# Kernel tuning notes

Measured on AMD Instinct MI355X. Metric: run time of the kernel, lower is better.

Reference implementation:

```python
import jax, jax.numpy as jnp
import numpy as np

T, N, I, H, OUT = 16, 4096, 4, 32, 1


def setup_inputs() -> dict:
    key = jax.random.key(0)
    ks = jax.random.split(key, 12)
    f32 = jnp.float32
    x_path = jax.random.normal(ks[0], (T, N, I), f32)
    adj = jax.random.normal(ks[1], (N, N), f32) / np.float32(np.sqrt(N))
    W_enc = jax.random.normal(ks[2], (I, H), f32) / np.float32(np.sqrt(I))
    b_enc = jnp.zeros((H,), f32)
    W_gcn = jax.random.normal(ks[3], (H, H), f32) / np.float32(np.sqrt(H))
    b_gcn = jnp.zeros((H,), f32)
    W_time = jax.random.normal(ks[4], (H, H), f32) / np.float32(np.sqrt(H))
    b_time = jnp.zeros((H,), f32)
    W_proj = jax.random.normal(ks[5], (H, H * I), f32) * np.float32(0.1 / np.sqrt(H))
    b_proj = jnp.zeros((H * I,), f32)
    W_d1 = jax.random.normal(ks[6], (H, 16), f32) / np.float32(np.sqrt(H))
    b_d1 = jnp.zeros((16,), f32)
    W_d2 = jax.random.normal(ks[7], (16, OUT), f32) / np.float32(4.0)
    b_d2 = jnp.zeros((OUT,), f32)
    return dict(x_path=x_path, adj=adj, W_enc=W_enc, b_enc=b_enc,
                W_gcn=W_gcn, b_gcn=b_gcn, W_time=W_time, b_time=b_time,
                W_proj=W_proj, b_proj=b_proj, W_d1=W_d1, b_d1=b_d1,
                W_d2=W_d2, b_d2=b_d2)


def _natural_cubic_coeffs(y):
    # y: (T, C) samples on uniform grid t=0..T-1 (h=1).
    # Natural cubic spline: tridiagonal solve for second derivatives M.
    Tn = y.shape[0]
    main = jnp.ones((Tn,), y.dtype).at[1:-1].set(4.0)
    A = jnp.diag(main)
    idx = jnp.arange(1, Tn - 1)
    A = A.at[idx, idx - 1].set(1.0).at[idx, idx + 1].set(1.0)
    rhs = jnp.zeros_like(y).at[1:-1].set(6.0 * (y[2:] - 2.0 * y[1:-1] + y[:-2]))
    M = jnp.linalg.solve(A, rhs)
    b = (y[1:] - y[:-1]) - (2.0 * M[:-1] + M[1:]) / 6.0
    c = M[:-1] / 2.0
    d = (M[1:] - M[:-1]) / 6.0
    return b, c, d  # each (T-1, C); dX/dt on interval i at local s: b+2cs+3ds^2


def reference(x_path, adj, W_enc, b_enc, W_gcn, b_gcn, W_time, b_time,
              W_proj, b_proj, W_d1, b_d1, W_d2, b_d2):
    Tn, Nn, In = x_path.shape
    Hn = W_enc.shape[1]
    y = x_path.reshape(Tn, Nn * In)
    sb, sc, sd = _natural_cubic_coeffs(y)

    # z0 = encoder(X(t0)); spline value at grid point 0 equals the sample.
    z0 = x_path[0] @ W_enc + b_enc  # (N, H)

    def vf(z, dxdt):
        # SpatialVectorField + projector + block-diagonal Jacobian applied to dX/dt.
        # z: (N, H), dxdt: (N, I)
        zn = adj @ z                                     # GCN neighbor aggregation
        h = jax.nn.relu(zn @ W_gcn + b_gcn + z @ W_time + b_time)
        sens = (h @ W_proj + b_proj).reshape(Nn, Hn, In)  # per-site Jacobian blocks
        # site_identity * sens -> block-diag; matmul with dX reduces to per-site contraction
        return jnp.einsum('nhi,ni->nh', sens, dxdt)

    def rk4_step(z, coefs):
        bi, ci, di = coefs  # (N*I,)
        def dxdt(s):
            return (bi + 2.0 * ci * s + 3.0 * di * s * s).reshape(Nn, In)
        k1 = vf(z, dxdt(0.0))
        k2 = vf(z + 0.5 * k1, dxdt(0.5))
        k3 = vf(z + 0.5 * k2, dxdt(0.5))
        k4 = vf(z + k3, dxdt(1.0))
        zn = z + (k1 + 2.0 * k2 + 2.0 * k3 + k4) / 6.0
        return zn, zn

    _, zs = jax.lax.scan(rk4_step, z0, (sb, sc, sd))
    zT = jnp.concatenate([z0[None], zs], axis=0)  # (T, N, H)

    hdec = jax.nn.relu(zT @ W_d1 + b_d1)
    return jax.nn.sigmoid(hdec @ W_d2 + b_d2)  # (T, N, OUT)
```

## Files before the change

kernel.cpp:

```cpp
#include <hip/hip_runtime.h>
#include <hip/hip_bf16.h>

#define NN 4096
#define NI 16384
#define HH 32

typedef __attribute__((ext_vector_type(8))) short short8;
typedef __attribute__((ext_vector_type(4))) float f32x4;

__device__ __forceinline__ short f2bs(float f) {
  __hip_bfloat16 b = __float2bfloat16(f);
  return *(short*)&b;
}

__global__ __launch_bounds__(512) void k_cvt(const float* __restrict__ a,
                                             short* __restrict__ ab) {
  const int tid = threadIdx.x;
  const int W = tid >> 6, lane = tid & 63;
  const int fr = lane & 15, oct = lane >> 4;
  const int R = blockIdx.x;
  const float* srow = a + (long)(R * 16 + fr) * NN + W * 512 + oct * 8;
  short* drow = ab + ((long)(R * 8 + W) * 16) * 512 + lane * 8;
#pragma unroll 4
  for (int i = 0; i < 16; ++i) {
    const float4 u0 = *(const float4*)(srow + i * 32);
    const float4 u1 = *(const float4*)(srow + i * 32 + 4);
    short8 r;
    r[0] = f2bs(u0.x); r[1] = f2bs(u0.y); r[2] = f2bs(u0.z); r[3] = f2bs(u0.w);
    r[4] = f2bs(u1.x); r[5] = f2bs(u1.y); r[6] = f2bs(u1.z); r[7] = f2bs(u1.w);
    *(short8*)(drow + i * 512) = r;
  }
}

__device__ __forceinline__ long zt_idx(int n, int h) {
  const int hb = h >> 4, hl = h & 15;
  const int kb = n >> 5, oct = (n >> 3) & 3, j = n & 7;
  return ((long)(hb * 128 + kb) * 64 + hl + 16 * oct) * 8 + j;
}

__global__ void k_spline(const float* __restrict__ x,
                         float* __restrict__ dx0, float* __restrict__ dxh,
                         float* __restrict__ dx1) {
  const int c = blockIdx.x * 256 + threadIdx.x;
  float y[16];
#pragma unroll
  for (int t = 0; t < 16; ++t) y[t] = x[t * NI + c];
  float cp[15], dp[15], M[16];
  cp[1] = 0.25f;
  dp[1] = (6.f * (y[2] - 2.f * y[1] + y[0])) * 0.25f;
#pragma unroll
  for (int i = 2; i <= 14; ++i) {
    float ri = 6.f * (y[i + 1] - 2.f * y[i] + y[i - 1]);
    float inv = 1.f / (4.f - cp[i - 1]);
    cp[i] = inv;
    dp[i] = (ri - dp[i - 1]) * inv;
  }
  M[0] = 0.f; M[15] = 0.f;
  M[14] = dp[14];
#pragma unroll
  for (int i = 13; i >= 1; --i) M[i] = dp[i] - cp[i] * M[i + 1];
#pragma unroll
  for (int i = 0; i < 15; ++i) {
    float b = (y[i + 1] - y[i]) - (2.f * M[i] + M[i + 1]) * (1.f / 6.f);
    float cc = 0.5f * M[i];
    float dd = (M[i + 1] - M[i]) * (1.f / 6.f);
    dx0[i * NI + c] = b;
    dxh[i * NI + c] = b + cc + 0.75f * dd;
    dx1[i * NI + c] = b + 2.f * cc + 3.f * dd;
  }
}

__global__ void k_enc(const float* __restrict__ x,
                      const float* __restrict__ We,
                      const float* __restrict__ be,
                      float* __restrict__ zcur, float* __restrict__ ze,
                      short* __restrict__ zT) {
  const int g = blockIdx.x * 256 + threadIdx.x;
  const int n = g >> 5, h = g & 31;
  float acc = be[h];
#pragma unroll
  for (int i = 0; i < 4; ++i) acc = fmaf(x[n * 4 + i], We[i * 32 + h], acc);
  zcur[g] = acc;
  ze[g] = acc;
  zT[zt_idx(n, h)] = f2bs(acc);
}

__global__ void k_dec0(const float* __restrict__ z,
                       const float* __restrict__ W1,
                       const float* __restrict__ b1,
                       const float* __restrict__ W2,
                       const float* __restrict__ b2,
                       float* __restrict__ out) {
  __shared__ float W1s[32][17];
  __shared__ float b1s[16], W2s[16], b2s;
  const int tid = threadIdx.x;
  for (int idx = tid; idx < 512; idx += 256) W1s[idx >> 4][idx & 15] = W1[idx];
  if (tid < 16) { b1s[tid] = b1[tid]; W2s[tid] = W2[tid]; }
  if (tid == 0) b2s = b2[0];
  __syncthreads();
  const int n = blockIdx.x * 256 + tid;
  const float* zr = z + (long)n * 32;
  float zv[32];
#pragma unroll
  for (int hh = 0; hh < 32; ++hh) zv[hh] = zr[hh];
  float acc = b2s;
#pragma unroll
  for (int jj = 0; jj < 16; ++jj) {
    float hv = b1s[jj];
#pragma unroll
    for (int hh = 0; hh < 32; ++hh) hv = fmaf(zv[hh], W1s[hh][jj], hv);
    acc = fmaf(fmaxf(hv, 0.f), W2s[jj], acc);
  }
  out[n] = 1.f / (1.f + expf(-acc));
}

__global__ __launch_bounds__(512) void k_vf(
    const short* __restrict__ adjb,
    const short* __restrict__ zT_in,
    short* __restrict__ zT_out,
    float* __restrict__ z_eval,
    const float* __restrict__ z_base,
    float* __restrict__ z_next,
    float* __restrict__ kout,
    const float* __restrict__ k1, const float* __restrict__ k2,
    const float* __restrict__ k3,
    const float* __restrict__ dxsel,
    const float* __restrict__ Wg, const float* __restrict__ bg,
    const float* __restrict__ Wt, const float* __restrict__ bt,
    const float* __restrict__ Wp, const float* __restrict__ bp,
    const float* __restrict__ Wd1, const float* __restrict__ bd1,
    const float* __restrict__ Wd2, const float* __restrict__ bd2,
    float* __restrict__ out, int out_base, int j) {
  __shared__ float red[8][16][32];
  __shared__ float zn_s[16][32];
  __shared__ float h_s[16][32];
  __shared__ float ze_s[16][32];
  __shared__ float Wg_s[32][32];
  __shared__ float Wt_s[32][32];
  __shared__ float Wp_s[32][132];
  __shared__ float Wd1_s[32][16];
  __shared__ float bgt_s[32];
  __shared__ float bp_s[128];
  __shared__ float dsm[33];

  const int tid = threadIdx.x;
  const int lane = tid & 63;
  const int w = tid >> 6;
  const int r0 = blockIdx.x * 16;

  for (int idx = tid; idx < 1024; idx += 512) {
    Wg_s[idx >> 5][idx & 31] = Wg[idx];
    Wt_s[idx >> 5][idx & 31] = Wt[idx];
  }
  for (int idx = tid; idx < 4096; idx += 512)
    Wp_s[idx >> 7][idx & 127] = Wp[idx];
  if (tid < 32) bgt_s[tid] = bg[tid] + bt[tid];
  if (tid < 128) bp_s[tid] = bp[tid];
  ze_s[tid >> 5][tid & 31] = z_eval[r0 * 32 + tid];
  if (j == 4) {
    Wd1_s[tid >> 4 & 31][tid & 15] = (tid < 512) ? Wd1[tid] : 0.f;
    if (tid < 16) { dsm[tid] = bd1[tid]; dsm[16 + tid] = Wd2[tid]; }
    if (tid == 0) dsm[32] = bd2[0];
  }

  f32x4 acc0 = {0.f, 0.f, 0.f, 0.f};
  f32x4 acc1 = {0.f, 0.f, 0.f, 0.f};
  const short* ap = adjb + ((long)(blockIdx.x * 8 + w) * 16) * 512 + lane * 8;
  const short* b0p = zT_in + ((long)(w * 16)) * 512 + lane * 8;
  const short* b1p = zT_in + ((long)(128 + w * 16)) * 512 + lane * 8;
#pragma unroll 8
  for (int i = 0; i < 16; ++i) {
    const short8 a  = *(const short8*)(ap + i * 512);
    const short8 b0 = *(const short8*)(b0p + i * 512);
    const short8 b1 = *(const short8*)(b1p + i * 512);
    acc0 = __builtin_amdgcn_mfma_f32_16x16x32_bf16(a, b0, acc0, 0, 0, 0);
    acc1 = __builtin_amdgcn_mfma_f32_16x16x32_bf16(a, b1, acc1, 0, 0, 0);
  }
  {
    const int crow = (lane >> 4) * 4;
    const int ccol = lane & 15;
#pragma unroll
    for (int q = 0; q < 4; ++q) {
      red[w][crow + q][ccol] = acc0[q];
      red[w][crow + q][ccol + 16] = acc1[q];
    }
  }
  __syncthreads();

  const int r = tid >> 5, c = tid & 31;
  {
    float zn = 0.f;
#pragma unroll
    for (int q = 0; q < 8; ++q) zn += red[q][r][c];
    zn_s[r][c] = zn;
  }
  __syncthreads();

  {
    float hv = bgt_s[c];
#pragma unroll
    for (int kk = 0; kk < 32; ++kk)
      hv = fmaf(zn_s[r][kk], Wg_s[kk][c], fmaf(ze_s[r][kk], Wt_s[kk][c], hv));
    h_s[r][c] = fmaxf(hv, 0.f);
  }
  __syncthreads();

  {
    const long row = r0 + r;
    float kv = 0.f;
#pragma unroll
    for (int i = 0; i < 4; ++i) {
      float s = bp_s[c * 4 + i];
#pragma unroll
      for (int hp = 0; hp < 32; ++hp) s = fmaf(h_s[r][hp], Wp_s[hp][c * 4 + i], s);
      kv = fmaf(s, dxsel[row * 4 + i], kv);
    }
    const long g = row * 32 + c;
    float znew;
    if (j == 4) {
      znew = z_base[g] + (k1[g] + 2.f * k2[g] + 2.f * k3[g] + kv) * (1.f / 6.f);
      z_next[g] = znew;
      zn_s[r][c] = znew;
    } else {
      kout[g] = kv;
      znew = z_base[g] + ((j == 3) ? 1.f : 0.5f) * kv;
    }
    z_eval[g] = znew;
    zT_out[zt_idx((int)row, c)] = f2bs(znew);
  }

  if (j == 4) {
    __syncthreads();
    if (tid < 16) {
      float acc = dsm[32];
#pragma unroll
      for (int jj = 0; jj < 16; ++jj) {
        float hv = dsm[jj];
#pragma unroll
        for (int hh = 0; hh < 32; ++hh) hv = fmaf(zn_s[tid][hh], Wd1_s[hh][jj], hv);
        acc = fmaf(fmaxf(hv, 0.f), dsm[16 + jj], acc);
      }
      out[out_base + r0 + tid] = 1.f / (1.f + expf(-acc));
    }
  }
}

extern "C" void kernel_launch(void* const* d_in, const int* in_sizes, int n_in,
                              void* d_out, int out_size, void* d_ws, size_t ws_size,
                              hipStream_t stream) {
  (void)in_sizes; (void)n_in; (void)out_size; (void)ws_size;
  const float* x      = (const float*)d_in[0];
  const float* adj    = (const float*)d_in[1];
  const float* W_enc  = (const float*)d_in[2];
  const float* b_enc  = (const float*)d_in[3];
  const float* W_gcn  = (const float*)d_in[4];
  const float* b_gcn  = (const float*)d_in[5];
  const float* W_time = (const float*)d_in[6];
  const float* b_time = (const float*)d_in[7];
  const float* W_proj = (const float*)d_in[8];
  const float* b_proj = (const float*)d_in[9];
  const float* W_d1   = (const float*)d_in[10];
  const float* b_d1   = (const float*)d_in[11];
  const float* W_d2   = (const float*)d_in[12];
  const float* b_d2   = (const float*)d_in[13];
  float* out = (float*)d_out;

  float* dx0   = (float*)d_ws;
  float* dxh   = dx0 + 15 * NI;
  float* dx1   = dxh + 15 * NI;
  float* zcur  = dx1 + 15 * NI;
  float* znext = zcur + NN * HH;
  float* zev   = znext + NN * HH;
  float* k1b   = zev + NN * HH;
  float* k2b   = k1b + NN * HH;
  float* k3b   = k2b + NN * HH;
  short* zTa   = (short*)(k3b + NN * HH);
  short* zTb   = zTa + HH * NN;
  short* adjb  = zTb + HH * NN;

  k_cvt<<<256, 512, 0, stream>>>(adj, adjb);
  k_spline<<<64, 256, 0, stream>>>(x, dx0, dxh, dx1);
  k_enc<<<512, 256, 0, stream>>>(x, W_enc, b_enc, zcur, zev, zTa);
  k_dec0<<<16, 256, 0, stream>>>(zcur, W_d1, b_d1, W_d2, b_d2, out);

  short* zin = zTa;
  short* zout = zTb;
  for (int t = 0; t < 15; ++t) {
    const float* ds[4] = { dx0 + t * NI, dxh + t * NI, dxh + t * NI, dx1 + t * NI };
    for (int j = 1; j <= 4; ++j) {
      float* ko = (j == 1) ? k1b : (j == 2) ? k2b : k3b;
      k_vf<<<256, 512, 0, stream>>>(adjb, zin, zout, zev, zcur, znext, ko,
                                    k1b, k2b, k3b, ds[j - 1],
                                    W_gcn, b_gcn, W_time, b_time, W_proj, b_proj,
                                    W_d1, b_d1, W_d2, b_d2, out, (t + 1) * NN, j);
      short* tmp = zin; zin = zout; zout = tmp;
    }
    float* tz = zcur; zcur = znext; znext = tz;
  }
}
```

Measured before the change: 810.4 us.

## Fuse all RK4 stages into one persistent cooperative kernel with grid barriers

Replaces the 60 per-stage kernel launches, along with the separate conversion, encoder and decoder kernels, with a single persistent cooperative kernel that loops over all stages. Stages are separated by a custom grid barrier built on atomic counters. Each block converts its 16 rows of the adjacency matrix to bf16 once and keeps them in LDS (128 KB) for the whole run. RK4 intermediates stay in registers instead of global buffers. This removes launch overhead and repeated adjacency reads from HBM, but adds barrier latency and reduces occupancy to one 256-thread block per CU.

```diff
diff --git a/kernel.cpp b/kernel.cpp
--- a/kernel.cpp
+++ b/kernel.cpp
@@ -12,24 +12,9 @@
   __hip_bfloat16 b = __float2bfloat16(f);
   return *(short*)&b;
 }
-
-__global__ __launch_bounds__(512) void k_cvt(const float* __restrict__ a,
-                                             short* __restrict__ ab) {
-  const int tid = threadIdx.x;
-  const int W = tid >> 6, lane = tid & 63;
-  const int fr = lane & 15, oct = lane >> 4;
-  const int R = blockIdx.x;
-  const float* srow = a + (long)(R * 16 + fr) * NN + W * 512 + oct * 8;
-  short* drow = ab + ((long)(R * 8 + W) * 16) * 512 + lane * 8;
-#pragma unroll 4
-  for (int i = 0; i < 16; ++i) {
-    const float4 u0 = *(const float4*)(srow + i * 32);
-    const float4 u1 = *(const float4*)(srow + i * 32 + 4);
-    short8 r;
-    r[0] = f2bs(u0.x); r[1] = f2bs(u0.y); r[2] = f2bs(u0.z); r[3] = f2bs(u0.w);
-    r[4] = f2bs(u1.x); r[5] = f2bs(u1.y); r[6] = f2bs(u1.z); r[7] = f2bs(u1.w);
-    *(short8*)(drow + i * 512) = r;
-  }
+__device__ __forceinline__ float bs2f(short s) {
+  __hip_bfloat16 b = *(__hip_bfloat16*)&s;
+  return __bfloat162float(b);
 }
 
 __device__ __forceinline__ long zt_idx(int n, int h) {
@@ -40,8 +25,9 @@
 
 __global__ void k_spline(const float* __restrict__ x,
                          float* __restrict__ dx0, float* __restrict__ dxh,
-                         float* __restrict__ dx1) {
+                         float* __restrict__ dx1, unsigned* __restrict__ bar) {
   const int c = blockIdx.x * 256 + threadIdx.x;
+  if (blockIdx.x == 0) { bar[threadIdx.x] = 0u; bar[threadIdx.x + 256] = 0u; }
   float y[16];
 #pragma unroll
   for (int t = 0; t < 16; ++t) y[t] = x[t * NI + c];
@@ -70,75 +56,49 @@
   }
 }
 
-__global__ void k_enc(const float* __restrict__ x,
-                      const float* __restrict__ We,
-                      const float* __restrict__ be,
-                      float* __restrict__ zcur, float* __restrict__ ze,
-                      short* __restrict__ zT) {
-  const int g = blockIdx.x * 256 + threadIdx.x;
-  const int n = g >> 5, h = g & 31;
-  float acc = be[h];
-#pragma unroll
-  for (int i = 0; i < 4; ++i) acc = fmaf(x[n * 4 + i], We[i * 32 + h], acc);
-  zcur[g] = acc;
-  ze[g] = acc;
-  zT[zt_idx(n, h)] = f2bs(acc);
-}
-
-__global__ void k_dec0(const float* __restrict__ z,
-                       const float* __restrict__ W1,
-                       const float* __restrict__ b1,
-                       const float* __restrict__ W2,
-                       const float* __restrict__ b2,
-                       float* __restrict__ out) {
-  __shared__ float W1s[32][17];
-  __shared__ float b1s[16], W2s[16], b2s;
-  const int tid = threadIdx.x;
-  for (int idx = tid; idx < 512; idx += 256) W1s[idx >> 4][idx & 15] = W1[idx];
-  if (tid < 16) { b1s[tid] = b1[tid]; W2s[tid] = W2[tid]; }
-  if (tid == 0) b2s = b2[0];
+struct OdeP {
+  const float *x, *We, *be, *adj;
+  const float *Wg, *bg, *Wt, *bt, *Wp, *bp, *Wd1, *bd1, *Wd2, *bd2;
+  const float *dx0, *dxh, *dx1;
+  short *zTa, *zTb;
+  float *out;
+  unsigned *bar;
+};
+
+__device__ __forceinline__ void gbar(const OdeP& p, int bar_i, int bid) {
   __syncthreads();
-  const int n = blockIdx.x * 256 + tid;
-  const float* zr = z + (long)n * 32;
-  float zv[32];
-#pragma unroll
-  for (int hh = 0; hh < 32; ++hh) zv[hh] = zr[hh];
-  float acc = b2s;
-#pragma unroll
-  for (int jj = 0; jj < 16; ++jj) {
-    float hv = b1s[jj];
-#pragma unroll
-    for (int hh = 0; hh < 32; ++hh) hv = fmaf(zv[hh], W1s[hh][jj], hv);
-    acc = fmaf(fmaxf(hv, 0.f), W2s[jj], acc);
-  }
-  out[n] = 1.f / (1.f + expf(-acc));
-}
-
-__global__ __launch_bounds__(512) void k_vf(
-    const short* __restrict__ adjb,
-    const short* __restrict__ zT_in,
-    short* __restrict__ zT_out,
-    float* __restrict__ z_eval,
-    const float* __restrict__ z_base,
-    float* __restrict__ z_next,
-    float* __restrict__ kout,
-    const float* __restrict__ k1, const float* __restrict__ k2,
-    const float* __restrict__ k3,
-    const float* __restrict__ dxsel,
-    const float* __restrict__ Wg, const float* __restrict__ bg,
-    const float* __restrict__ Wt, const float* __restrict__ bt,
-    const float* __restrict__ Wp, const float* __restrict__ bp,
-    const float* __restrict__ Wd1, const float* __restrict__ bd1,
-    const float* __restrict__ Wd2, const float* __restrict__ bd2,
-    float* __restrict__ out, int out_base, int j) {
-  __shared__ float red[8][16][32];
-  __shared__ float zn_s[16][32];
-  __shared__ float h_s[16][32];
-  __shared__ float ze_s[16][32];
+  if (threadIdx.x == 0) {
+    __threadfence();
+    __hip_atomic_fetch_add(&p.bar[(bid & 7) * 32], 1u,
+                           __ATOMIC_RELAXED, __HIP_MEMORY_SCOPE_AGENT);
+    const unsigned tgt = (unsigned)(bar_i + 1);
+    if (bid == 0) {
+#pragma unroll 1
+      for (int s2 = 0; s2 < 8; ++s2)
+        while (__hip_atomic_load(&p.bar[s2 * 32], __ATOMIC_RELAXED,
+                                 __HIP_MEMORY_SCOPE_AGENT) < tgt * 32u)
+          __builtin_amdgcn_s_sleep(1);
+      __threadfence();
+      __hip_atomic_store(&p.bar[256], tgt, __ATOMIC_RELAXED, __HIP_MEMORY_SCOPE_AGENT);
+    } else {
+      while (__hip_atomic_load(&p.bar[256], __ATOMIC_RELAXED,
+                               __HIP_MEMORY_SCOPE_AGENT) < tgt)
+        __builtin_amdgcn_s_sleep(1);
+    }
+  }
+  __syncthreads();
+  __threadfence();
+}
+
+__global__ __launch_bounds__(256, 1) void k_ode(OdeP p) {
+  __shared__ __align__(16) short adjs[65536];
+  __shared__ float zn_s[16][33];
+  __shared__ float ze_s[16][33];
+  __shared__ float h_s[16][33];
   __shared__ float Wg_s[32][32];
   __shared__ float Wt_s[32][32];
-  __shared__ float Wp_s[32][132];
-  __shared__ float Wd1_s[32][16];
+  __shared__ float Wp_s[32][128];
+  __shared__ short Wd1_s[512];
   __shared__ float bgt_s[32];
   __shared__ float bp_s[128];
   __shared__ float dsm[33];
@@ -146,102 +106,173 @@
   const int tid = threadIdx.x;
   const int lane = tid & 63;
   const int w = tid >> 6;
-  const int r0 = blockIdx.x * 16;
-
-  for (int idx = tid; idx < 1024; idx += 512) {
-    Wg_s[idx >> 5][idx & 31] = Wg[idx];
-    Wt_s[idx >> 5][idx & 31] = Wt[idx];
-  }
-  for (int idx = tid; idx < 4096; idx += 512)
-    Wp_s[idx >> 7][idx & 127] = Wp[idx];
-  if (tid < 32) bgt_s[tid] = bg[tid] + bt[tid];
-  if (tid < 128) bp_s[tid] = bp[tid];
-  ze_s[tid >> 5][tid & 31] = z_eval[r0 * 32 + tid];
-  if (j == 4) {
-    Wd1_s[tid >> 4 & 31][tid & 15] = (tid < 512) ? Wd1[tid] : 0.f;
-    if (tid < 16) { dsm[tid] = bd1[tid]; dsm[16 + tid] = Wd2[tid]; }
-    if (tid == 0) dsm[32] = bd2[0];
-  }
-
-  f32x4 acc0 = {0.f, 0.f, 0.f, 0.f};
-  f32x4 acc1 = {0.f, 0.f, 0.f, 0.f};
-  const short* ap = adjb + ((long)(blockIdx.x * 8 + w) * 16) * 512 + lane * 8;
-  const short* b0p = zT_in + ((long)(w * 16)) * 512 + lane * 8;
-  const short* b1p = zT_in + ((long)(128 + w * 16)) * 512 + lane * 8;
-#pragma unroll 8
-  for (int i = 0; i < 16; ++i) {
-    const short8 a  = *(const short8*)(ap + i * 512);
-    const short8 b0 = *(const short8*)(b0p + i * 512);
-    const short8 b1 = *(const short8*)(b1p + i * 512);
-    acc0 = __builtin_amdgcn_mfma_f32_16x16x32_bf16(a, b0, acc0, 0, 0, 0);
-    acc1 = __builtin_amdgcn_mfma_f32_16x16x32_bf16(a, b1, acc1, 0, 0, 0);
-  }
+  const int bid = blockIdx.x;
+  const int r0 = bid * 16;
+  const int lane8 = lane * 8;
+  const int fr = lane & 15, oct = lane >> 4;
+
+  for (int idx = tid; idx < 1024; idx += 256) {
+    Wg_s[idx >> 5][idx & 31] = p.Wg[idx];
+    Wt_s[idx >> 5][idx & 31] = p.Wt[idx];
+  }
+  for (int idx = tid; idx < 4096; idx += 256) ((float*)Wp_s)[idx] = p.Wp[idx];
+  for (int idx = tid; idx < 512; idx += 256) Wd1_s[idx] = f2bs(p.Wd1[idx]);
+  if (tid < 32) bgt_s[tid] = p.bg[tid] + p.bt[tid];
+  if (tid < 128) bp_s[tid] = p.bp[tid];
+  if (tid < 16) { dsm[tid] = p.bd1[tid]; dsm[16 + tid] = p.Wd2[tid]; }
+  if (tid == 0) dsm[32] = p.bd2[0];
+
   {
-    const int crow = (lane >> 4) * 4;
-    const int ccol = lane & 15;
-#pragma unroll
-    for (int q = 0; q < 4; ++q) {
-      red[w][crow + q][ccol] = acc0[q];
-      red[w][crow + q][ccol + 16] = acc1[q];
-    }
+    const float* srow = p.adj + (long)(r0 + fr) * NN + w * 1024 + oct * 8;
+#pragma unroll 4
+    for (int i = 0; i < 32; ++i) {
+      const float4 u0 = *(const float4*)(srow + i * 32);
+      const float4 u1 = *(const float4*)(srow + i * 32 + 4);
+      short8 r;
+      r[0] = f2bs(u0.x); r[1] = f2bs(u0.y); r[2] = f2bs(u0.z); r[3] = f2bs(u0.w);
+      r[4] = f2bs(u1.x); r[5] = f2bs(u1.y); r[6] = f2bs(u1.z); r[7] = f2bs(u1.w);
+      *(short8*)&adjs[(w * 32 + i) * 512 + lane8] = r;
+    }
+  }
+
+  float zb[2], k1r[2] = {0.f, 0.f}, k2r[2] = {0.f, 0.f}, k3r[2] = {0.f, 0.f};
+#pragma unroll
+  for (int e = 0; e < 2; ++e) {
+    const int idx = tid + e * 256;
+    const int r = idx >> 5, c = idx & 31;
+    const int n = r0 + r;
+    const float4 xv = *(const float4*)&p.x[n * 4];
+    float z0 = p.be[c];
+    z0 = fmaf(xv.x, p.We[0 * 32 + c], z0);
+    z0 = fmaf(xv.y, p.We[1 * 32 + c], z0);
+    z0 = fmaf(xv.z, p.We[2 * 32 + c], z0);
+    z0 = fmaf(xv.w, p.We[3 * 32 + c], z0);
+    zb[e] = z0;
+    ze_s[r][c] = z0;
+    h_s[r][c] = z0;
+    zn_s[r][c] = 0.f;
+    p.zTa[zt_idx(n, c)] = f2bs(z0);
   }
   __syncthreads();
 
-  const int r = tid >> 5, c = tid & 31;
-  {
-    float zn = 0.f;
-#pragma unroll
-    for (int q = 0; q < 8; ++q) zn += red[q][r][c];
-    zn_s[r][c] = zn;
-  }
-  __syncthreads();
-
-  {
-    float hv = bgt_s[c];
-#pragma unroll
-    for (int kk = 0; kk < 32; ++kk)
-      hv = fmaf(zn_s[r][kk], Wg_s[kk][c], fmaf(ze_s[r][kk], Wt_s[kk][c], hv));
-    h_s[r][c] = fmaxf(hv, 0.f);
-  }
-  __syncthreads();
-
-  {
-    const long row = r0 + r;
-    float kv = 0.f;
-#pragma unroll
-    for (int i = 0; i < 4; ++i) {
-      float s = bp_s[c * 4 + i];
-#pragma unroll
-      for (int hp = 0; hp < 32; ++hp) s = fmaf(h_s[r][hp], Wp_s[hp][c * 4 + i], s);
-      kv = fmaf(s, dxsel[row * 4 + i], kv);
-    }
-    const long g = row * 32 + c;
-    float znew;
+  if (tid < 16) {
+    float acc = dsm[32];
+#pragma unroll
+    for (int jj = 0; jj < 16; ++jj) {
+      float hv = dsm[jj];
+#pragma unroll
+      for (int hh = 0; hh < 32; ++hh) hv = fmaf(h_s[tid][hh], bs2f(Wd1_s[hh * 16 + jj]), hv);
+      acc = fmaf(fmaxf(hv, 0.f), dsm[16 + jj], acc);
+    }
+    p.out[r0 + tid] = 1.f / (1.f + expf(-acc));
+  }
+
+  int bar_i = 0;
+  gbar(p, bar_i++, bid);
+
+  const int fb = w * 32;
+#pragma unroll 1
+  for (int s = 0; s < 60; ++s) {
+    const int t = s >> 2;
+    const int j = (s & 3) + 1;
+    const short* zi = (s & 1) ? p.zTb : p.zTa;
+    short* zo = (s & 1) ? p.zTa : p.zTb;
+    const float* dxp = (j == 1) ? (p.dx0 + t * NI)
+                     : (j == 4) ? (p.dx1 + t * NI) : (p.dxh + t * NI);
+
+    f32x4 a0 = {0.f,0.f,0.f,0.f}, a1 = {0.f,0.f,0.f,0.f};
+    f32x4 a2 = {0.f,0.f,0.f,0.f}, a3 = {0.f,0.f,0.f,0.f};
+#pragma unroll 4
+    for (int i = 0; i < 32; i += 2) {
+      const int f0 = fb + i, f1 = fb + i + 1;
+      const short8 av0 = *(const short8*)&adjs[f0 * 512 + lane8];
+      const short8 bv00 = *(const short8*)(zi + (long)f0 * 512 + lane8);
+      const short8 bv01 = *(const short8*)(zi + (long)(128 + f0) * 512 + lane8);
+      const short8 av1 = *(const short8*)&adjs[f1 * 512 + lane8];
+      const short8 bv10 = *(const short8*)(zi + (long)f1 * 512 + lane8);
+      const short8 bv11 = *(const short8*)(zi + (long)(128 + f1) * 512 + lane8);
+      a0 = __builtin_amdgcn_mfma_f32_16x16x32_bf16(av0, bv00, a0, 0, 0, 0);
+      a1 = __builtin_amdgcn_mfma_f32_16x16x32_bf16(av0, bv01, a1, 0, 0, 0);
+      a2 = __builtin_amdgcn_mfma_f32_16x16x32_bf16(av1, bv10, a2, 0, 0, 0);
+      a3 = __builtin_amdgcn_mfma_f32_16x16x32_bf16(av1, bv11, a3, 0, 0, 0);
+    }
+    const f32x4 acc0 = a0 + a2, acc1 = a1 + a3;
+    {
+      const int crow = (lane >> 4) * 4;
+      const int ccol = lane & 15;
+#pragma unroll
+      for (int q = 0; q < 4; ++q) {
+        atomicAdd(&zn_s[crow + q][ccol], acc0[q]);
+        atomicAdd(&zn_s[crow + q][ccol + 16], acc1[q]);
+      }
+    }
+    __syncthreads();
+
+#pragma unroll
+    for (int e = 0; e < 2; ++e) {
+      const int idx = tid + e * 256;
+      const int r = idx >> 5, c = idx & 31;
+      float hv = bgt_s[c];
+#pragma unroll
+      for (int kk = 0; kk < 32; ++kk)
+        hv = fmaf(zn_s[r][kk], Wg_s[kk][c], fmaf(ze_s[r][kk], Wt_s[kk][c], hv));
+      h_s[r][c] = fmaxf(hv, 0.f);
+    }
+    __syncthreads();
+
+    float znew[2];
+#pragma unroll
+    for (int e = 0; e < 2; ++e) {
+      const int idx = tid + e * 256;
+      const int r = idx >> 5, c = idx & 31;
+      const int row = r0 + r;
+      const float4 dxv = *(const float4*)&dxp[row * 4];
+      float kv = 0.f;
+#pragma unroll
+      for (int i = 0; i < 4; ++i) {
+        float sv = bp_s[c * 4 + i];
+#pragma unroll
+        for (int hp = 0; hp < 32; ++hp) sv = fmaf(h_s[r][hp], Wp_s[hp][c * 4 + i], sv);
+        const float dx = (i == 0) ? dxv.x : (i == 1) ? dxv.y : (i == 2) ? dxv.z : dxv.w;
+        kv = fmaf(sv, dx, kv);
+      }
+      float zn2;
+      if (j == 4) {
+        zn2 = zb[e] + (k1r[e] + 2.f * k2r[e] + 2.f * k3r[e] + kv) * (1.f / 6.f);
+        zb[e] = zn2;
+      } else {
+        if (j == 1) k1r[e] = kv; else if (j == 2) k2r[e] = kv; else k3r[e] = kv;
+        zn2 = zb[e] + ((j == 3) ? 1.f : 0.5f) * kv;
+      }
+      znew[e] = zn2;
+      zn_s[r][c] = 0.f;
+      ze_s[r][c] = zn2;
+      zo[zt_idx(row, c)] = f2bs(zn2);
+    }
+
     if (j == 4) {
-      znew = z_base[g] + (k1[g] + 2.f * k2[g] + 2.f * k3[g] + kv) * (1.f / 6.f);
-      z_next[g] = znew;
-      zn_s[r][c] = znew;
-    } else {
-      kout[g] = kv;
-      znew = z_base[g] + ((j == 3) ? 1.f : 0.5f) * kv;
-    }
-    z_eval[g] = znew;
-    zT_out[zt_idx((int)row, c)] = f2bs(znew);
-  }
-
-  if (j == 4) {
-    __syncthreads();
-    if (tid < 16) {
-      float acc = dsm[32];
-#pragma unroll
-      for (int jj = 0; jj < 16; ++jj) {
-        float hv = dsm[jj];
-#pragma unroll
-        for (int hh = 0; hh < 32; ++hh) hv = fmaf(zn_s[tid][hh], Wd1_s[hh][jj], hv);
-        acc = fmaf(fmaxf(hv, 0.f), dsm[16 + jj], acc);
-      }
-      out[out_base + r0 + tid] = 1.f / (1.f + expf(-acc));
-    }
+      __syncthreads();
+#pragma unroll
+      for (int e = 0; e < 2; ++e) {
+        const int idx = tid + e * 256;
+        h_s[idx >> 5][idx & 31] = znew[e];
+      }
+      __syncthreads();
+      if (tid < 16) {
+        float acc = dsm[32];
+#pragma unroll
+        for (int jj = 0; jj < 16; ++jj) {
+          float hv = dsm[jj];
+#pragma unroll
+          for (int hh = 0; hh < 32; ++hh)
+            hv = fmaf(h_s[tid][hh], bs2f(Wd1_s[hh * 16 + jj]), hv);
+          acc = fmaf(fmaxf(hv, 0.f), dsm[16 + jj], acc);
+        }
+        p.out[(t + 1) * NN + r0 + tid] = 1.f / (1.f + expf(-acc));
+      }
+    }
+
+    if (s < 59) gbar(p, bar_i++, bid);
   }
 }
 
@@ -263,38 +294,29 @@
   const float* b_d1   = (const float*)d_in[11];
   const float* W_d2   = (const float*)d_in[12];
   const float* b_d2   = (const float*)d_in[13];
-  float* out = (float*)d_out;
-
-  float* dx0   = (float*)d_ws;
-  float* dxh   = dx0 + 15 * NI;
-  float* dx1   = dxh + 15 * NI;
-  float* zcur  = dx1 + 15 * NI;
-  float* znext = zcur + NN * HH;
-  float* zev   = znext + NN * HH;
-  float* k1b   = zev + NN * HH;
-  float* k2b   = k1b + NN * HH;
-  float* k3b   = k2b + NN * HH;
-  short* zTa   = (short*)(k3b + NN * HH);
-  short* zTb   = zTa + HH * NN;
-  short* adjb  = zTb + HH * NN;
-
-  k_cvt<<<256, 512, 0, stream>>>(adj, adjb);
-  k_spline<<<64, 256, 0, stream>>>(x, dx0, dxh, dx1);
-  k_enc<<<512, 256, 0, stream>>>(x, W_enc, b_enc, zcur, zev, zTa);
-  k_dec0<<<16, 256, 0, stream>>>(zcur, W_d1, b_d1, W_d2, b_d2, out);
-
-  short* zin = zTa;
-  short* zout = zTb;
-  for (int t = 0; t < 15; ++t) {
-    const float* ds[4] = { dx0 + t * NI, dxh + t * NI, dxh + t * NI, dx1 + t * NI };
-    for (int j = 1; j <= 4; ++j) {
-      float* ko = (j == 1) ? k1b : (j == 2) ? k2b : k3b;
-      k_vf<<<256, 512, 0, stream>>>(adjb, zin, zout, zev, zcur, znext, ko,
-                                    k1b, k2b, k3b, ds[j - 1],
-                                    W_gcn, b_gcn, W_time, b_time, W_proj, b_proj,
-                                    W_d1, b_d1, W_d2, b_d2, out, (t + 1) * NN, j);
-      short* tmp = zin; zin = zout; zout = tmp;
-    }
-    float* tz = zcur; zcur = znext; znext = tz;
-  }
-}
+
+  unsigned* bar = (unsigned*)d_ws;
+  float* dx0 = (float*)(bar + 512);
+  float* dxh = dx0 + 15 * NI;
+  float* dx1 = dxh + 15 * NI;
+  short* zTa = (short*)(dx1 + 15 * NI);
+  short* zTb = zTa + HH * NN;
+
+  k_spline<<<64, 256, 0, stream>>>(x, dx0, dxh, dx1, bar);
+
+  OdeP p;
+  p.x = x; p.We = W_enc; p.be = b_enc; p.adj = adj;
+  p.Wg = W_gcn; p.bg = b_gcn; p.Wt = W_time; p.bt = b_time;
+  p.Wp = W_proj; p.bp = b_proj; p.Wd1 = W_d1; p.bd1 = b_d1;
+  p.Wd2 = W_d2; p.bd2 = b_d2;
+  p.dx0 = dx0; p.dxh = dxh; p.dx1 = dx1;
+  p.zTa = zTa; p.zTb = zTb;
+  p.out = (float*)d_out; p.bar = bar;
+
+  void* args[] = { &p };
+  hipError_t rc = hipLaunchCooperativeKernel((const void*)k_ode, dim3(256), dim3(256),
+                                             args, 0, stream);
+  if (rc != hipSuccess) {
+    k_ode<<<256, 256, 0, stream>>>(p);
+  }
+}
```

After: 2.304 ms. 2.84x slower.

## Double k_vf block to 16 waves, issue MFMA loads before weight staging

Applied to the files above, without the earlier changes.

The vector-field kernel now launches 1024 threads per block, so 16 waves each handle half as many K-chunks of the adjacency matmul, and the partial results are reduced through a padded shared buffer. The adjacency and state loads are issued before the weight staging to shared memory, so the global latency overlaps with it. The projection stage now loads h into registers and reads Wp as float4. The intent is to hide memory latency in this latency-bound, launch-heavy step. The cost is a larger reduction and half of the threads sitting idle in the epilogue stages.

```diff
diff --git a/kernel.cpp b/kernel.cpp
--- a/kernel.cpp
+++ b/kernel.cpp
@@ -114,7 +114,7 @@
   out[n] = 1.f / (1.f + expf(-acc));
 }
 
-__global__ __launch_bounds__(512) void k_vf(
+__global__ __launch_bounds__(1024) void k_vf(
     const short* __restrict__ adjb,
     const short* __restrict__ zT_in,
     short* __restrict__ zT_out,
@@ -131,13 +131,13 @@
     const float* __restrict__ Wd1, const float* __restrict__ bd1,
     const float* __restrict__ Wd2, const float* __restrict__ bd2,
     float* __restrict__ out, int out_base, int j) {
-  __shared__ float red[8][16][32];
-  __shared__ float zn_s[16][32];
-  __shared__ float h_s[16][32];
-  __shared__ float ze_s[16][32];
+  __shared__ float red2[16][32][17];
+  __shared__ float zn_s[16][33];
+  __shared__ float h_s[16][33];
+  __shared__ float ze_s[16][33];
   __shared__ float Wg_s[32][32];
   __shared__ float Wt_s[32][32];
-  __shared__ float Wp_s[32][132];
+  __shared__ float Wp_s[32][136];
   __shared__ float Wd1_s[32][16];
   __shared__ float bgt_s[32];
   __shared__ float bp_s[128];
@@ -147,56 +147,62 @@
   const int lane = tid & 63;
   const int w = tid >> 6;
   const int r0 = blockIdx.x * 16;
-
-  for (int idx = tid; idx < 1024; idx += 512) {
-    Wg_s[idx >> 5][idx & 31] = Wg[idx];
-    Wt_s[idx >> 5][idx & 31] = Wt[idx];
-  }
-  for (int idx = tid; idx < 4096; idx += 512)
+  const int lane8 = lane * 8;
+
+  f32x4 a0 = {0.f,0.f,0.f,0.f}, a1 = {0.f,0.f,0.f,0.f};
+  const short* ap  = adjb + ((long)(blockIdx.x * 128 + w * 8)) * 512 + lane8;
+  const short* b0p = zT_in + ((long)(w * 8)) * 512 + lane8;
+  const short* b1p = zT_in + ((long)(128 + w * 8)) * 512 + lane8;
+#pragma unroll
+  for (int i = 0; i < 8; ++i) {
+    const short8 av = *(const short8*)(ap + i * 512);
+    const short8 b0 = *(const short8*)(b0p + i * 512);
+    const short8 b1 = *(const short8*)(b1p + i * 512);
+    a0 = __builtin_amdgcn_mfma_f32_16x16x32_bf16(av, b0, a0, 0, 0, 0);
+    a1 = __builtin_amdgcn_mfma_f32_16x16x32_bf16(av, b1, a1, 0, 0, 0);
+  }
+
+  for (int idx = tid; idx < 1024; idx += 1024) { }
+  if (tid < 1024) {
+    if (tid < 512) {
+      Wg_s[tid >> 5][tid & 31] = Wg[tid];
+      Wt_s[tid >> 5][tid & 31] = Wt[tid];
+    } else {
+      const int q = tid - 512;
+      Wg_s[(q + 512) >> 5][q & 31] = Wg[512 + q];
+      Wt_s[(q + 512) >> 5][q & 31] = Wt[512 + q];
+    }
+  }
+  for (int idx = tid; idx < 4096; idx += 1024)
     Wp_s[idx >> 7][idx & 127] = Wp[idx];
+  if (tid < 512) Wd1_s[tid >> 4][tid & 15] = Wd1[tid];
   if (tid < 32) bgt_s[tid] = bg[tid] + bt[tid];
   if (tid < 128) bp_s[tid] = bp[tid];
-  ze_s[tid >> 5][tid & 31] = z_eval[r0 * 32 + tid];
-  if (j == 4) {
-    Wd1_s[tid >> 4 & 31][tid & 15] = (tid < 512) ? Wd1[tid] : 0.f;
-    if (tid < 16) { dsm[tid] = bd1[tid]; dsm[16 + tid] = Wd2[tid]; }
-    if (tid == 0) dsm[32] = bd2[0];
-  }
-
-  f32x4 acc0 = {0.f, 0.f, 0.f, 0.f};
-  f32x4 acc1 = {0.f, 0.f, 0.f, 0.f};
-  const short* ap = adjb + ((long)(blockIdx.x * 8 + w) * 16) * 512 + lane * 8;
-  const short* b0p = zT_in + ((long)(w * 16)) * 512 + lane * 8;
-  const short* b1p = zT_in + ((long)(128 + w * 16)) * 512 + lane * 8;
-#pragma unroll 8
-  for (int i = 0; i < 16; ++i) {
-    const short8 a  = *(const short8*)(ap + i * 512);
-    const short8 b0 = *(const short8*)(b0p + i * 512);
-    const short8 b1 = *(const short8*)(b1p + i * 512);
-    acc0 = __builtin_amdgcn_mfma_f32_16x16x32_bf16(a, b0, acc0, 0, 0, 0);
-    acc1 = __builtin_amdgcn_mfma_f32_16x16x32_bf16(a, b1, acc1, 0, 0, 0);
-  }
+  if (tid < 512) ze_s[tid >> 5][tid & 31] = z_eval[r0 * 32 + tid];
+  if (tid < 16) { dsm[tid] = bd1[tid]; dsm[16 + tid] = Wd2[tid]; }
+  if (tid == 0) dsm[32] = bd2[0];
+
   {
     const int crow = (lane >> 4) * 4;
     const int ccol = lane & 15;
 #pragma unroll
     for (int q = 0; q < 4; ++q) {
-      red[w][crow + q][ccol] = acc0[q];
-      red[w][crow + q][ccol + 16] = acc1[q];
+      red2[crow + q][ccol][w] = a0[q];
+      red2[crow + q][ccol + 16][w] = a1[q];
     }
   }
   __syncthreads();
 
-  const int r = tid >> 5, c = tid & 31;
-  {
+  const int r = (tid >> 5) & 15, c = tid & 31;
+  if (tid < 512) {
     float zn = 0.f;
 #pragma unroll
-    for (int q = 0; q < 8; ++q) zn += red[q][r][c];
+    for (int q = 0; q < 16; ++q) zn += red2[r][c][q];
     zn_s[r][c] = zn;
   }
   __syncthreads();
 
-  {
+  if (tid < 512) {
     float hv = bgt_s[c];
 #pragma unroll
     for (int kk = 0; kk < 32; ++kk)
@@ -205,31 +211,38 @@
   }
   __syncthreads();
 
-  {
-    const long row = r0 + r;
-    float kv = 0.f;
-#pragma unroll
-    for (int i = 0; i < 4; ++i) {
-      float s = bp_s[c * 4 + i];
-#pragma unroll
-      for (int hp = 0; hp < 32; ++hp) s = fmaf(h_s[r][hp], Wp_s[hp][c * 4 + i], s);
-      kv = fmaf(s, dxsel[row * 4 + i], kv);
-    }
-    const long g = row * 32 + c;
-    float znew;
+  float znew = 0.f;
+  if (tid < 512) {
+    const int row = r0 + r;
+    float hr[32];
+#pragma unroll
+    for (int hp = 0; hp < 32; ++hp) hr[hp] = h_s[r][hp];
+    float s0 = bp_s[c * 4], s1 = bp_s[c * 4 + 1], s2 = bp_s[c * 4 + 2], s3 = bp_s[c * 4 + 3];
+#pragma unroll
+    for (int hp = 0; hp < 32; ++hp) {
+      const float4 wv = *(const float4*)&Wp_s[hp][c * 4];
+      s0 = fmaf(hr[hp], wv.x, s0);
+      s1 = fmaf(hr[hp], wv.y, s1);
+      s2 = fmaf(hr[hp], wv.z, s2);
+      s3 = fmaf(hr[hp], wv.w, s3);
+    }
+    const float4 dxv = *(const float4*)&dxsel[row * 4];
+    const float kv = s0 * dxv.x + s1 * dxv.y + s2 * dxv.z + s3 * dxv.w;
+    const long g = (long)row * 32 + c;
     if (j == 4) {
       znew = z_base[g] + (k1[g] + 2.f * k2[g] + 2.f * k3[g] + kv) * (1.f / 6.f);
       z_next[g] = znew;
-      zn_s[r][c] = znew;
     } else {
       kout[g] = kv;
       znew = z_base[g] + ((j == 3) ? 1.f : 0.5f) * kv;
     }
     z_eval[g] = znew;
-    zT_out[zt_idx((int)row, c)] = f2bs(znew);
+    zT_out[zt_idx(row, c)] = f2bs(znew);
   }
 
   if (j == 4) {
+    __syncthreads();
+    if (tid < 512) zn_s[r][c] = znew;
     __syncthreads();
     if (tid < 16) {
       float acc = dsm[32];
@@ -289,10 +302,10 @@
     const float* ds[4] = { dx0 + t * NI, dxh + t * NI, dxh + t * NI, dx1 + t * NI };
     for (int j = 1; j <= 4; ++j) {
       float* ko = (j == 1) ? k1b : (j == 2) ? k2b : k3b;
-      k_vf<<<256, 512, 0, stream>>>(adjb, zin, zout, zev, zcur, znext, ko,
-                                    k1b, k2b, k3b, ds[j - 1],
-                                    W_gcn, b_gcn, W_time, b_time, W_proj, b_proj,
-                                    W_d1, b_d1, W_d2, b_d2, out, (t + 1) * NN, j);
+      k_vf<<<256, 1024, 0, stream>>>(adjb, zin, zout, zev, zcur, znext, ko,
+                                     k1b, k2b, k3b, ds[j - 1],
+                                     W_gcn, b_gcn, W_time, b_time, W_proj, b_proj,
+                                     W_d1, b_d1, W_d2, b_d2, out, (t + 1) * NN, j);
       short* tmp = zin; zin = zout; zout = tmp;
     }
     float* tz = zcur; zcur = znext; znext = tz;
```

New measurement: 783.7 us. 3.3% less time.
